# Optimization experiments

Measured on AMD Instinct MI355X. Metric: run time of the kernel, lower is better.

Reference implementation:

```python
import jax, jax.numpy as jnp
import numpy as np

D_MODEL = 768
N_HEADS = 4
D_HEAD = D_MODEL // N_HEADS
EPS = 1e-3  # keras LayerNormalization default


def gelu_tanh(x):
    return 0.5 * x * (1.0 + jnp.tanh(np.sqrt(2.0 / np.pi) * (x + 0.044715 * x ** 3)))


def layer_norm(x, g, b):
    mu = jnp.mean(x, axis=-1, keepdims=True)
    var = jnp.mean(jnp.square(x - mu), axis=-1, keepdims=True)
    return (x - mu) * jax.lax.rsqrt(var + EPS) * g + b


def setup_inputs() -> dict:
    key = jax.random.key(0)
    ks = jax.random.split(key, 12)
    B, S = 8, 1024
    x = jax.random.normal(ks[0], (B, S, D_MODEL), dtype=jnp.float32)
    # causal mask: 1 on strictly-future positions (added as mask * -1e9)
    mask = jnp.triu(jnp.ones((S, S), dtype=jnp.float32), k=1)[None, None]
    s = 0.02
    params = {
        'W1': jax.random.normal(ks[1], (D_MODEL, 3 * D_MODEL)) * s,
        'b1': jnp.zeros((3 * D_MODEL,), jnp.float32),
        'W3': jax.random.normal(ks[2], (D_MODEL, D_MODEL)) * s,
        'b3': jnp.zeros((D_MODEL,), jnp.float32),
        'W2': jax.random.normal(ks[3], (D_MODEL, 4 * D_MODEL)) * s,
        'b2': jnp.zeros((4 * D_MODEL,), jnp.float32),
        'W4': jax.random.normal(ks[4], (4 * D_MODEL, D_MODEL)) * s,
        'b4': jnp.zeros((D_MODEL,), jnp.float32),
        'g1': jnp.ones((D_MODEL,), jnp.float32),
        'be1': jnp.zeros((D_MODEL,), jnp.float32),
        'g2': jnp.ones((D_MODEL,), jnp.float32),
        'be2': jnp.zeros((D_MODEL,), jnp.float32),
    }
    return {'x': x, 'mask': mask, **params}


def reference(x, mask, W1, b1, W3, b3, W2, b2, W4, b4, g1, be1, g2, be2):
    B, S, _ = x.shape
    xn = layer_norm(x, g1, be1)
    qkv = xn @ W1 + b1                                  # [B,S,3D]
    q, k, v = jnp.split(qkv, 3, axis=-1)
    def split_heads(t):
        return t.reshape(B, S, N_HEADS, D_HEAD).transpose(0, 2, 1, 3)  # [B,H,S,dh]
    q, k, v = map(split_heads, (q, k, v))
    present = jnp.stack([k, v], axis=1)                  # [B,2,H,S,dh]
    w = jnp.einsum('bhqd,bhkd->bhqk', q, k)
    # NOTE: source divides by rsqrt(d_head) => multiplies by sqrt(d_head) (faithful bug)
    w = w * jnp.sqrt(jnp.float32(D_HEAD))
    w = w + mask * -1e9
    w = jax.nn.softmax(w, axis=-1)
    attn = jnp.einsum('bhqk,bhkd->bhqd', w, v)           # [B,H,S,dh]
    attn = attn.transpose(0, 2, 1, 3).reshape(B, S, D_MODEL)
    x = attn @ W3 + b3 + x                               # residual 1
    xn2 = layer_norm(x, g2, be2)
    h = gelu_tanh(xn2 @ W2 + b2)                         # [B,S,4D]
    x = h @ W4 + b4 + x                                  # residual 2
    return x, present
```

## Files before the change

kernel.cpp:

```cpp
#include <hip/hip_runtime.h>
#include <hip/hip_bf16.h>
#include <cstdint>

#define D_MODEL 768
#define NH 4
#define DH 192
#define SEQ 1024
#define BATCH 8

typedef __bf16 bf16x8 __attribute__((ext_vector_type(8)));
typedef float floatx4 __attribute__((ext_vector_type(4)));

__device__ __forceinline__ float bf2f(ushort u) {
    union { uint32_t i; float f; } x; x.i = ((uint32_t)u) << 16; return x.f;
}
__device__ __forceinline__ ushort f2bf(float f) {
    union { float f; uint32_t i; } x; x.f = f;
    uint32_t i = x.i;
    uint32_t r = (i + 0x7FFFu + ((i >> 16) & 1u)) >> 16;
    return (ushort)r;
}

__device__ __forceinline__ void gl_lds16(const void* g, void* l) {
    __builtin_amdgcn_global_load_lds(
        (const __attribute__((address_space(1))) uint32_t*)g,
        (__attribute__((address_space(3))) uint32_t*)l, 16, 0, 0);
}

template <int SPLIT>
__global__ void ln_kernel(const float* __restrict__ x, const float* __restrict__ g,
                          const float* __restrict__ be,
                          ushort* __restrict__ y_hi, ushort* __restrict__ y_lo) {
    int row = blockIdx.x;
    int tid = threadIdx.x;
    const float* xr = x + (size_t)row * D_MODEL;
    float v[3];
    float s = 0.f, ss = 0.f;
#pragma unroll
    for (int i = 0; i < 3; i++) {
        float t = xr[tid + i * 256];
        v[i] = t; s += t; ss += t * t;
    }
#pragma unroll
    for (int off = 32; off > 0; off >>= 1) {
        s += __shfl_down(s, off);
        ss += __shfl_down(ss, off);
    }
    __shared__ float rs[4], rss[4];
    int wid = tid >> 6;
    if ((tid & 63) == 0) { rs[wid] = s; rss[wid] = ss; }
    __syncthreads();
    s = rs[0] + rs[1] + rs[2] + rs[3];
    ss = rss[0] + rss[1] + rss[2] + rss[3];
    float mu = s * (1.f / 768.f);
    float var = ss * (1.f / 768.f) - mu * mu;
    float rstd = rsqrtf(var + 1e-3f);
#pragma unroll
    for (int i = 0; i < 3; i++) {
        int d = tid + i * 256;
        float val = (v[i] - mu) * rstd * g[d] + be[d];
        ushort hi = f2bf(val);
        y_hi[(size_t)row * D_MODEL + d] = hi;
        if (SPLIT) y_lo[(size_t)row * D_MODEL + d] = f2bf(val - bf2f(hi));
    }
}

__global__ void transpose_kernel(const float* __restrict__ W, ushort* __restrict__ Wt,
                                 int K, int N) {
    __shared__ ushort tile[64][65];
    int nt = N >> 6;
    int bk = blockIdx.x / nt, bn = blockIdx.x % nt;
    int tid = threadIdx.x;
#pragma unroll
    for (int i = 0; i < 16; i++) {
        int lin = i * 256 + tid; int r = lin >> 6, c = lin & 63;
        tile[r][c] = f2bf(W[(size_t)(bk * 64 + r) * N + bn * 64 + c]);
    }
    __syncthreads();
#pragma unroll
    for (int i = 0; i < 16; i++) {
        int lin = i * 256 + tid; int r = lin >> 6, c = lin & 63;
        Wt[(size_t)(bn * 64 + r) * K + bk * 64 + c] = tile[c][r];
    }
}

__global__ void transpose_split_kernel(const float* __restrict__ W,
                                       ushort* __restrict__ Wt_hi, ushort* __restrict__ Wt_lo,
                                       int K, int N) {
    __shared__ ushort th[64][65];
    __shared__ ushort tl[64][65];
    int nt = N >> 6;
    int bk = blockIdx.x / nt, bn = blockIdx.x % nt;
    int tid = threadIdx.x;
#pragma unroll
    for (int i = 0; i < 16; i++) {
        int lin = i * 256 + tid; int r = lin >> 6, c = lin & 63;
        float v = W[(size_t)(bk * 64 + r) * N + bn * 64 + c];
        ushort hi = f2bf(v);
        th[r][c] = hi;
        tl[r][c] = f2bf(v - bf2f(hi));
    }
    __syncthreads();
#pragma unroll
    for (int i = 0; i < 16; i++) {
        int lin = i * 256 + tid; int r = lin >> 6, c = lin & 63;
        size_t o = (size_t)(bn * 64 + r) * K + bk * 64 + c;
        Wt_hi[o] = th[c][r];
        Wt_lo[o] = tl[c][r];
    }
}

__global__ __launch_bounds__(256, 2) void gemm_qkv_split(
    const ushort* __restrict__ Ah, const ushort* __restrict__ Al,
    const ushort* __restrict__ Bh, const ushort* __restrict__ Bl,
    const float* __restrict__ bias,
    float* __restrict__ Qf, float* __restrict__ present,
    ushort* __restrict__ Khg, ushort* __restrict__ Klg, ushort* __restrict__ Vtg) {
    const int K = 768;
    __shared__ __align__(16) __bf16 sAh[2][128][32];
    __shared__ __align__(16) __bf16 sAl[2][128][32];
    __shared__ __align__(16) __bf16 sBh[2][128][32];
    __shared__ __align__(16) __bf16 sBl[2][128][32];
    int tid = threadIdx.x;
    int rowBase = blockIdx.y << 7;
    int colBase = blockIdx.x << 7;
    int wave = tid >> 6, lane = tid & 63;
    int wm = (wave & 1) << 6, wn = (wave >> 1) << 6;
    int lrow = lane & 15, q = lane >> 4;
    int lkswz = ((q ^ ((lrow >> 1) & 3)) << 3);
    floatx4 acc[4][4] = {};

    int srow = lane >> 2;
    int schunk = (lane & 3) ^ ((lane >> 3) & 3);
    const ushort* Ah0 = Ah + (size_t)(rowBase + wave * 32 + srow) * K + schunk * 8;
    const ushort* Al0 = Al + (size_t)(rowBase + wave * 32 + srow) * K + schunk * 8;
    const ushort* Bh0 = Bh + (size_t)(colBase + wave * 32 + srow) * K + schunk * 8;
    const ushort* Bl0 = Bl + (size_t)(colBase + wave * 32 + srow) * K + schunk * 8;
    const size_t r16 = (size_t)16 * K;
    int wr = wave * 32;

    gl_lds16(Ah0, &sAh[0][wr][0]);       gl_lds16(Ah0 + r16, &sAh[0][wr + 16][0]);
    gl_lds16(Al0, &sAl[0][wr][0]);       gl_lds16(Al0 + r16, &sAl[0][wr + 16][0]);
    gl_lds16(Bh0, &sBh[0][wr][0]);       gl_lds16(Bh0 + r16, &sBh[0][wr + 16][0]);
    gl_lds16(Bl0, &sBl[0][wr][0]);       gl_lds16(Bl0 + r16, &sBl[0][wr + 16][0]);
    __syncthreads();

    const int nt = K >> 5;
    for (int t = 0; t < nt; t++) {
        int cur = t & 1, nb = cur ^ 1;
        if (t + 1 < nt) {
            int k0 = (t + 1) << 5;
            gl_lds16(Ah0 + k0, &sAh[nb][wr][0]);  gl_lds16(Ah0 + r16 + k0, &sAh[nb][wr + 16][0]);
            gl_lds16(Al0 + k0, &sAl[nb][wr][0]);  gl_lds16(Al0 + r16 + k0, &sAl[nb][wr + 16][0]);
            gl_lds16(Bh0 + k0, &sBh[nb][wr][0]);  gl_lds16(Bh0 + r16 + k0, &sBh[nb][wr + 16][0]);
            gl_lds16(Bl0 + k0, &sBl[nb][wr][0]);  gl_lds16(Bl0 + r16 + k0, &sBl[nb][wr + 16][0]);
        }
        bf16x8 afh[4], afl[4], bvh[4], bvl[4];
#pragma unroll
        for (int i = 0; i < 4; i++) {
            afh[i] = *(const bf16x8*)&sAh[cur][wm + i * 16 + lrow][lkswz];
            afl[i] = *(const bf16x8*)&sAl[cur][wm + i * 16 + lrow][lkswz];
        }
#pragma unroll
        for (int jj = 0; jj < 4; jj++) {
            bvh[jj] = *(const bf16x8*)&sBh[cur][wn + jj * 16 + lrow][lkswz];
            bvl[jj] = *(const bf16x8*)&sBl[cur][wn + jj * 16 + lrow][lkswz];
        }
#pragma unroll
        for (int i = 0; i < 4; i++)
#pragma unroll
            for (int jj = 0; jj < 4; jj++) {
                acc[i][jj] = __builtin_amdgcn_mfma_f32_16x16x32_bf16(afh[i], bvh[jj], acc[i][jj], 0, 0, 0);
                acc[i][jj] = __builtin_amdgcn_mfma_f32_16x16x32_bf16(afh[i], bvl[jj], acc[i][jj], 0, 0, 0);
                acc[i][jj] = __builtin_amdgcn_mfma_f32_16x16x32_bf16(afl[i], bvh[jj], acc[i][jj], 0, 0, 0);
            }
        __syncthreads();
    }

    int cr = (lane >> 4) << 2;
    int cc = lane & 15;
#pragma unroll
    for (int jj = 0; jj < 4; jj++) {
        int col = colBase + wn + jj * 16 + cc;
        float bvs = bias[col];
        if (colBase < 768) {
#pragma unroll
            for (int i = 0; i < 4; i++) {
                int row0 = rowBase + wm + i * 16 + cr;
#pragma unroll
                for (int r = 0; r < 4; r++)
                    Qf[(size_t)(row0 + r) * 768 + col] = acc[i][jj][r] + bvs;
            }
        } else if (colBase < 1536) {
            int kc = col - 768;
            int h = kc / DH, d = kc - h * DH;
#pragma unroll
            for (int i = 0; i < 4; i++) {
                int row0 = rowBase + wm + i * 16 + cr;
#pragma unroll
                for (int r = 0; r < 4; r++) {
                    int row = row0 + r;
                    int b = row >> 10, s = row & 1023;
                    float v = acc[i][jj][r] + bvs;
                    present[((size_t)((b * 2) * NH + h) * SEQ + s) * DH + d] = v;
                    ushort hi = f2bf(v);
                    Khg[(size_t)row * 768 + kc] = hi;
                    Klg[(size_t)row * 768 + kc] = f2bf(v - bf2f(hi));
                }
            }
        } else {
            int vc = col - 1536;
            int h = vc / DH, d = vc - h * DH;
#pragma unroll
            for (int i = 0; i < 4; i++) {
                int row0 = rowBase + wm + i * 16 + cr;
#pragma unroll
                for (int r = 0; r < 4; r++) {
                    int row = row0 + r;
                    int b = row >> 10, s = row & 1023;
                    float v = acc[i][jj][r] + bvs;
                    present[((size_t)((b * 2 + 1) * NH + h) * SEQ + s) * DH + d] = v;
                    Vtg[((size_t)b * 768 + vc) * 1024 + s] = f2bf(v);
                }
            }
        }
    }
}

template <int GELU, int RES, int OUTF32>
__global__ __launch_bounds__(256, 4) void gemm_bt(
    const ushort* __restrict__ A, const ushort* __restrict__ Bt,
    const float* __restrict__ bias, const float* __restrict__ resid,
    void* __restrict__ Cout, int M, int N, int K) {
    __shared__ __align__(16) __bf16 sA[2][128][32];
    __shared__ __align__(16) __bf16 sB[2][128][32];
    int tid = threadIdx.x;
    int rowBase = blockIdx.y << 7;
    int colBase = blockIdx.x << 7;
    int wave = tid >> 6, lane = tid & 63;
    int wm = (wave & 1) << 6, wn = (wave >> 1) << 6;
    int lrow = lane & 15, q = lane >> 4;
    int lkswz = ((q ^ ((lrow >> 1) & 3)) << 3);
    floatx4 acc[4][4] = {};

    int srow = lane >> 2;
    int schunk = (lane & 3) ^ ((lane >> 3) & 3);
    const ushort* Ag0 = A + (size_t)(rowBase + wave * 32 + srow) * K + schunk * 8;
    const ushort* Bg0 = Bt + (size_t)(colBase + wave * 32 + srow) * K + schunk * 8;
    const size_t r16 = (size_t)16 * K;
    int wr = wave * 32;

    gl_lds16(Ag0, &sA[0][wr][0]);  gl_lds16(Ag0 + r16, &sA[0][wr + 16][0]);
    gl_lds16(Bg0, &sB[0][wr][0]);  gl_lds16(Bg0 + r16, &sB[0][wr + 16][0]);
    __syncthreads();

    int nt = K >> 5;
    for (int t = 0; t < nt; t++) {
        int cur = t & 1, nb = cur ^ 1;
        if (t + 1 < nt) {
            int k0 = (t + 1) << 5;
            gl_lds16(Ag0 + k0, &sA[nb][wr][0]);  gl_lds16(Ag0 + r16 + k0, &sA[nb][wr + 16][0]);
            gl_lds16(Bg0 + k0, &sB[nb][wr][0]);  gl_lds16(Bg0 + r16 + k0, &sB[nb][wr + 16][0]);
        }
        bf16x8 af[4], bv[4];
#pragma unroll
        for (int i = 0; i < 4; i++) af[i] = *(const bf16x8*)&sA[cur][wm + i * 16 + lrow][lkswz];
#pragma unroll
        for (int jj = 0; jj < 4; jj++) bv[jj] = *(const bf16x8*)&sB[cur][wn + jj * 16 + lrow][lkswz];
#pragma unroll
        for (int i = 0; i < 4; i++)
#pragma unroll
            for (int jj = 0; jj < 4; jj++)
                acc[i][jj] = __builtin_amdgcn_mfma_f32_16x16x32_bf16(af[i], bv[jj], acc[i][jj], 0, 0, 0);
        __syncthreads();
    }
    int cr = (lane >> 4) << 2;
    int cc = lane & 15;
#pragma unroll
    for (int jj = 0; jj < 4; jj++) {
        int col = colBase + wn + jj * 16 + cc;
        float bvs = bias[col];
#pragma unroll
        for (int i = 0; i < 4; i++) {
            int row0 = rowBase + wm + i * 16 + cr;
#pragma unroll
            for (int r = 0; r < 4; r++) {
                int row = row0 + r;
                float v = acc[i][jj][r] + bvs;
                if (GELU) {
                    float u = v;
                    float z2 = -1.5957691216057308f * (u + 0.044715f * u * u * u);
                    v = u / (1.f + __expf(z2));
                }
                if (RES) v += resid[(size_t)row * N + col];
                if (OUTF32) ((float*)Cout)[(size_t)row * N + col] = v;
                else ((ushort*)Cout)[(size_t)row * N + col] = f2bf(v);
            }
        }
    }
}

__global__ __launch_bounds__(512, 2) void attn_flash(
    const float* __restrict__ Qf, const ushort* __restrict__ Khg,
    const ushort* __restrict__ Klg, const ushort* __restrict__ Vtg,
    ushort* __restrict__ attn2) {
    int bi = blockIdx.x;
    int j = bi & 7;
    int h = (bi >> 3) & 3;
    int b = bi >> 5;
    int tid = threadIdx.x;
    int wave = tid >> 6, lane = tid & 63;
    int l15 = lane & 15, quad = lane >> 4;
    int tile = (wave < 4) ? (15 - j) : j;
    int w16 = wave & 3;
    int s0 = tile << 6;
    int its = 2 * (15 - j) + 2;
    int myKt = (s0 + w16 * 16 + 15) >> 5;

    __shared__ __align__(16) __bf16 sKh[2][32][200];
    __shared__ __align__(16) __bf16 sKl[2][32][200];
    __shared__ __align__(16) __bf16 sVt[2][192][40];
    __shared__ __align__(16) ushort sP[8][16][40];

    const bool lo_half = (tid < 256);
    const int kr0 = tid / 24, ke0 = (tid % 24) * 8;
    const int c1 = lo_half ? (512 + tid) : (256 + tid);
    const int kr1 = c1 / 24, ke1 = (c1 % 24) * 8;
    const int vd0 = tid >> 2, ve0 = (tid & 3) * 8;
    const int vd1 = (512 + tid) >> 2, ve1 = ((512 + tid) & 3) * 8;

    const ushort* Khb = Khg + (size_t)(b * 1024) * 768 + h * 192;
    const ushort* Klb = Klg + (size_t)(b * 1024) * 768 + h * 192;
    const ushort* Vtb = Vtg + ((size_t)(b * 768) + h * 192) * 1024;
    const ushort* Bb = lo_half ? Khb : Klb;
    __bf16* pKB = lo_half ? &sKh[0][kr1][ke1] : &sKl[0][kr1][ke1];

    uint4 rA, rB, rC, rD, rE;

    rA = *(const uint4*)(Khb + (size_t)kr0 * 768 + ke0);
    rC = *(const uint4*)(Klb + (size_t)kr0 * 768 + ke0);
    rB = *(const uint4*)(Bb + (size_t)kr1 * 768 + ke1);
    rD = *(const uint4*)(Vtb + (size_t)vd0 * 1024 + ve0);
    if (lo_half) rE = *(const uint4*)(Vtb + (size_t)vd1 * 1024 + ve1);

    bf16x8 qh[6], ql[6];
    {
        int qrow = s0 + w16 * 16 + l15;
        const float* qp = Qf + (size_t)(b * SEQ + qrow) * 768 + h * DH + quad * 8;
#pragma unroll
        for (int dt = 0; dt < 6; dt++) {
            float4 v0 = *(const float4*)(qp + dt * 32);
            float4 v1 = *(const float4*)(qp + dt * 32 + 4);
            float vv[8] = {v0.x, v0.y, v0.z, v0.w, v1.x, v1.y, v1.z, v1.w};
            bf16x8 hh, ll;
#pragma unroll
            for (int jj = 0; jj < 8; jj++) {
                float sv = vv[jj] * 13.856406460551018f;
                ushort hu = f2bf(sv);
                ((ushort*)&hh)[jj] = hu;
                ((ushort*)&ll)[jj] = f2bf(sv - bf2f(hu));
            }
            qh[dt] = hh; ql[dt] = ll;
        }
    }

    floatx4 O[12] = {};
    float m_run[4], l_run[4];
#pragma unroll
    for (int r = 0; r < 4; r++) { m_run[r] = -1e30f; l_run[r] = 0.f; }

    *(uint4*)&sKh[0][kr0][ke0] = rA;
    *(uint4*)&sKl[0][kr0][ke0] = rC;
    *(uint4*)(pKB) = rB;
    *(uint4*)&sVt[0][vd0][ve0] = rD;
    if (lo_half) *(uint4*)&sVt[0][vd1][ve1] = rE;
    __syncthreads();

    for (int kt = 0; kt < its; kt++) {
        int cur = kt & 1;
        bool pfetch = (kt + 1 < its);
        if (pfetch) {
            int koff = (kt + 1) * 32;
            rA = *(const uint4*)(Khb + (size_t)(koff + kr0) * 768 + ke0);
            rC = *(const uint4*)(Klb + (size_t)(koff + kr0) * 768 + ke0);
            rB = *(const uint4*)(Bb + (size_t)(koff + kr1) * 768 + ke1);
            rD = *(const uint4*)(Vtb + (size_t)vd0 * 1024 + koff + ve0);
            if (lo_half) rE = *(const uint4*)(Vtb + (size_t)vd1 * 1024 + koff + ve1);
        }
        if (kt <= myKt) {
            floatx4 S0 = {}, S1 = {};
#pragma unroll
            for (int dt = 0; dt < 6; dt++) {
                bf16x8 k0h = *(const bf16x8*)&sKh[cur][l15][dt * 32 + quad * 8];
                bf16x8 k0l = *(const bf16x8*)&sKl[cur][l15][dt * 32 + quad * 8];
                bf16x8 k1h = *(const bf16x8*)&sKh[cur][16 + l15][dt * 32 + quad * 8];
                bf16x8 k1l = *(const bf16x8*)&sKl[cur][16 + l15][dt * 32 + quad * 8];
                S0 = __builtin_amdgcn_mfma_f32_16x16x32_bf16(qh[dt], k0h, S0, 0, 0, 0);
                S0 = __builtin_amdgcn_mfma_f32_16x16x32_bf16(qh[dt], k0l, S0, 0, 0, 0);
                S0 = __builtin_amdgcn_mfma_f32_16x16x32_bf16(ql[dt], k0h, S0, 0, 0, 0);
                S1 = __builtin_amdgcn_mfma_f32_16x16x32_bf16(qh[dt], k1h, S1, 0, 0, 0);
                S1 = __builtin_amdgcn_mfma_f32_16x16x32_bf16(qh[dt], k1l, S1, 0, 0, 0);
                S1 = __builtin_amdgcn_mfma_f32_16x16x32_bf16(ql[dt], k1h, S1, 0, 0, 0);
            }
            int qg = s0 + w16 * 16 + quad * 4;
            int colb = kt * 32 + l15;
            float mt[4];
#pragma unroll
            for (int r = 0; r < 4; r++) {
                float a = (colb <= qg + r) ? S0[r] : -1e30f;
                float c = (colb + 16 <= qg + r) ? S1[r] : -1e30f;
                S0[r] = a; S1[r] = c;
                mt[r] = fmaxf(a, c);
            }
#pragma unroll
            for (int m = 1; m <= 8; m <<= 1)
#pragma unroll
                for (int r = 0; r < 4; r++) mt[r] = fmaxf(mt[r], __shfl_xor(mt[r], m));
            float alpha[4], rsum[4], P0[4], P1[4];
#pragma unroll
            for (int r = 0; r < 4; r++) {
                float mn = fmaxf(m_run[r], mt[r]);
                alpha[r] = __expf(m_run[r] - mn);
                m_run[r] = mn;
                P0[r] = __expf(S0[r] - mn);
                P1[r] = __expf(S1[r] - mn);
                rsum[r] = P0[r] + P1[r];
            }
#pragma unroll
            for (int m = 1; m <= 8; m <<= 1)
#pragma unroll
                for (int r = 0; r < 4; r++) rsum[r] += __shfl_xor(rsum[r], m);
#pragma unroll
            for (int r = 0; r < 4; r++) l_run[r] = l_run[r] * alpha[r] + rsum[r];
#pragma unroll
            for (int t = 0; t < 12; t++)
#pragma unroll
                for (int r = 0; r < 4; r++) O[t][r] *= alpha[r];
#pragma unroll
            for (int r = 0; r < 4; r++) {
                sP[wave][quad * 4 + r][l15]      = f2bf(P0[r]);
                sP[wave][quad * 4 + r][16 + l15] = f2bf(P1[r]);
            }
            bf16x8 pfrag = *(const bf16x8*)&sP[wave][l15][quad * 8];
#pragma unroll
            for (int t = 0; t < 12; t++) {
                bf16x8 vf = *(const bf16x8*)&sVt[cur][t * 16 + l15][quad * 8];
                O[t] = __builtin_amdgcn_mfma_f32_16x16x32_bf16(pfrag, vf, O[t], 0, 0, 0);
            }
        }
        if (pfetch) {
            int nb = cur ^ 1;
            *(uint4*)&sKh[nb][kr0][ke0] = rA;
            *(uint4*)&sKl[nb][kr0][ke0] = rC;
            *(uint4*)(pKB + nb * 6400) = rB;
            *(uint4*)&sVt[nb][vd0][ve0] = rD;
            if (lo_half) *(uint4*)&sVt[nb][vd1][ve1] = rE;
        }
        __syncthreads();
    }

    float inv[4];
#pragma unroll
    for (int r = 0; r < 4; r++) inv[r] = 1.f / l_run[r];
    int qrow = s0 + w16 * 16 + quad * 4;
#pragma unroll
    for (int t = 0; t < 12; t++)
#pragma unroll
        for (int r = 0; r < 4; r++)
            attn2[(size_t)(b * SEQ + qrow + r) * D_MODEL + h * DH + t * 16 + l15] =
                f2bf(O[t][r] * inv[r]);
}

extern "C" void kernel_launch(void* const* d_in, const int* in_sizes, int n_in,
                              void* d_out, int out_size, void* d_ws, size_t ws_size,
                              hipStream_t stream) {
    const float* x  = (const float*)d_in[0];
    const float* W1 = (const float*)d_in[2];
    const float* b1 = (const float*)d_in[3];
    const float* W3 = (const float*)d_in[4];
    const float* b3 = (const float*)d_in[5];
    const float* W2 = (const float*)d_in[6];
    const float* b2 = (const float*)d_in[7];
    const float* W4 = (const float*)d_in[8];
    const float* b4 = (const float*)d_in[9];
    const float* g1 = (const float*)d_in[10];
    const float* be1 = (const float*)d_in[11];
    const float* g2 = (const float*)d_in[12];
    const float* be2 = (const float*)d_in[13];

    char* ws = (char*)d_ws;
    ushort* W1t_hi = (ushort*)(ws + 0);
    ushort* W1t_lo = (ushort*)(ws + 3538944);
    ushort* W3t    = (ushort*)(ws + 7077888);
    ushort* W2t    = (ushort*)(ws + 8257536);
    ushort* W4t    = (ushort*)(ws + 12976128);
    ushort* xn_hi  = (ushort*)(ws + 17694720);
    ushort* attn2  = (ushort*)(ws + 17694720);
    ushort* xn_lo  = (ushort*)(ws + 30277632);
    ushort* xn2    = (ushort*)(ws + 30277632);
    float*  Qf     = (float*)(ws + 42860544);
    ushort* hbuf   = (ushort*)(ws + 42860544);
    ushort* Khg    = (ushort*)(ws + 68026368);
    ushort* Klg    = (ushort*)(ws + 80609280);
    ushort* Vtg    = (ushort*)(ws + 93192192);
    float*  x1     = (float*)(ws + 105775104);

    float* out0 = (float*)d_out;
    float* present = out0 + 6291456;

    transpose_split_kernel<<<(768 / 64) * (2304 / 64), 256, 0, stream>>>(W1, W1t_hi, W1t_lo, 768, 2304);
    transpose_kernel<<<(768 / 64) * (768 / 64), 256, 0, stream>>>(W3, W3t, 768, 768);
    transpose_kernel<<<(768 / 64) * (3072 / 64), 256, 0, stream>>>(W2, W2t, 768, 3072);
    transpose_kernel<<<(3072 / 64) * (768 / 64), 256, 0, stream>>>(W4, W4t, 3072, 768);

    ln_kernel<1><<<8192, 256, 0, stream>>>(x, g1, be1, xn_hi, xn_lo);
    gemm_qkv_split<<<dim3(2304 / 128, 8192 / 128), 256, 0, stream>>>(
        xn_hi, xn_lo, W1t_hi, W1t_lo, b1, Qf, present, Khg, Klg, Vtg);
    attn_flash<<<BATCH * NH * 8, 512, 0, stream>>>(Qf, Khg, Klg, Vtg, attn2);
    gemm_bt<0, 1, 1><<<dim3(768 / 128, 8192 / 128), 256, 0, stream>>>(
        attn2, W3t, b3, x, x1, 8192, 768, 768);
    ln_kernel<0><<<8192, 256, 0, stream>>>(x1, g2, be2, xn2, nullptr);
    gemm_bt<1, 0, 0><<<dim3(3072 / 128, 8192 / 128), 256, 0, stream>>>(
        xn2, W2t, b2, nullptr, hbuf, 8192, 3072, 768);
    gemm_bt<0, 1, 1><<<dim3(768 / 128, 8192 / 128), 256, 0, stream>>>(
        hbuf, W4t, b4, x1, out0, 8192, 768, 3072);
}
```

Measured before the change: 513.1 us.

## Single-buffer QKV GEMM for higher occupancy, emit split bf16 Q directly

The QKV GEMM drops LDS double buffering in favour of a single buffer with syncs around each load, and raises launch bounds from 2 to 4 blocks per CU so latency is hidden by more resident waves instead of prefetch. The GEMM epilogue now writes Q as hi/lo bf16 pairs rather than fp32, and the sqrt(d_head) scale moves from Q onto K. The attention kernel then loads ready-made bf16x8 Q fragments instead of converting fp32. This trades explicit load/compute overlap and possible register pressure under the tighter bound for occupancy and less Q traffic and conversion work.

```diff
diff --git a/kernel.cpp b/kernel.cpp
--- a/kernel.cpp
+++ b/kernel.cpp
@@ -110,17 +110,17 @@
     }
 }
 
-__global__ __launch_bounds__(256, 2) void gemm_qkv_split(
+__global__ __launch_bounds__(256, 4) void gemm_qkv_split(
     const ushort* __restrict__ Ah, const ushort* __restrict__ Al,
     const ushort* __restrict__ Bh, const ushort* __restrict__ Bl,
     const float* __restrict__ bias,
-    float* __restrict__ Qf, float* __restrict__ present,
+    ushort* __restrict__ Qhg, ushort* __restrict__ Qlg, float* __restrict__ present,
     ushort* __restrict__ Khg, ushort* __restrict__ Klg, ushort* __restrict__ Vtg) {
     const int K = 768;
-    __shared__ __align__(16) __bf16 sAh[2][128][32];
-    __shared__ __align__(16) __bf16 sAl[2][128][32];
-    __shared__ __align__(16) __bf16 sBh[2][128][32];
-    __shared__ __align__(16) __bf16 sBl[2][128][32];
+    __shared__ __align__(16) __bf16 sAh[128][32];
+    __shared__ __align__(16) __bf16 sAl[128][32];
+    __shared__ __align__(16) __bf16 sBh[128][32];
+    __shared__ __align__(16) __bf16 sBl[128][32];
     int tid = threadIdx.x;
     int rowBase = blockIdx.y << 7;
     int colBase = blockIdx.x << 7;
@@ -139,32 +139,25 @@
     const size_t r16 = (size_t)16 * K;
     int wr = wave * 32;
 
-    gl_lds16(Ah0, &sAh[0][wr][0]);       gl_lds16(Ah0 + r16, &sAh[0][wr + 16][0]);
-    gl_lds16(Al0, &sAl[0][wr][0]);       gl_lds16(Al0 + r16, &sAl[0][wr + 16][0]);
-    gl_lds16(Bh0, &sBh[0][wr][0]);       gl_lds16(Bh0 + r16, &sBh[0][wr + 16][0]);
-    gl_lds16(Bl0, &sBl[0][wr][0]);       gl_lds16(Bl0 + r16, &sBl[0][wr + 16][0]);
-    __syncthreads();
-
     const int nt = K >> 5;
     for (int t = 0; t < nt; t++) {
-        int cur = t & 1, nb = cur ^ 1;
-        if (t + 1 < nt) {
-            int k0 = (t + 1) << 5;
-            gl_lds16(Ah0 + k0, &sAh[nb][wr][0]);  gl_lds16(Ah0 + r16 + k0, &sAh[nb][wr + 16][0]);
-            gl_lds16(Al0 + k0, &sAl[nb][wr][0]);  gl_lds16(Al0 + r16 + k0, &sAl[nb][wr + 16][0]);
-            gl_lds16(Bh0 + k0, &sBh[nb][wr][0]);  gl_lds16(Bh0 + r16 + k0, &sBh[nb][wr + 16][0]);
-            gl_lds16(Bl0 + k0, &sBl[nb][wr][0]);  gl_lds16(Bl0 + r16 + k0, &sBl[nb][wr + 16][0]);
-        }
+        if (t) __syncthreads();
+        int k0 = t << 5;
+        gl_lds16(Ah0 + k0, &sAh[wr][0]);  gl_lds16(Ah0 + r16 + k0, &sAh[wr + 16][0]);
+        gl_lds16(Al0 + k0, &sAl[wr][0]);  gl_lds16(Al0 + r16 + k0, &sAl[wr + 16][0]);
+        gl_lds16(Bh0 + k0, &sBh[wr][0]);  gl_lds16(Bh0 + r16 + k0, &sBh[wr + 16][0]);
+        gl_lds16(Bl0 + k0, &sBl[wr][0]);  gl_lds16(Bl0 + r16 + k0, &sBl[wr + 16][0]);
+        __syncthreads();
         bf16x8 afh[4], afl[4], bvh[4], bvl[4];
 #pragma unroll
         for (int i = 0; i < 4; i++) {
-            afh[i] = *(const bf16x8*)&sAh[cur][wm + i * 16 + lrow][lkswz];
-            afl[i] = *(const bf16x8*)&sAl[cur][wm + i * 16 + lrow][lkswz];
+            afh[i] = *(const bf16x8*)&sAh[wm + i * 16 + lrow][lkswz];
+            afl[i] = *(const bf16x8*)&sAl[wm + i * 16 + lrow][lkswz];
         }
 #pragma unroll
         for (int jj = 0; jj < 4; jj++) {
-            bvh[jj] = *(const bf16x8*)&sBh[cur][wn + jj * 16 + lrow][lkswz];
-            bvl[jj] = *(const bf16x8*)&sBl[cur][wn + jj * 16 + lrow][lkswz];
+            bvh[jj] = *(const bf16x8*)&sBh[wn + jj * 16 + lrow][lkswz];
+            bvl[jj] = *(const bf16x8*)&sBl[wn + jj * 16 + lrow][lkswz];
         }
 #pragma unroll
         for (int i = 0; i < 4; i++)
@@ -174,7 +167,6 @@
                 acc[i][jj] = __builtin_amdgcn_mfma_f32_16x16x32_bf16(afh[i], bvl[jj], acc[i][jj], 0, 0, 0);
                 acc[i][jj] = __builtin_amdgcn_mfma_f32_16x16x32_bf16(afl[i], bvh[jj], acc[i][jj], 0, 0, 0);
             }
-        __syncthreads();
     }
 
     int cr = (lane >> 4) << 2;
@@ -188,8 +180,12 @@
             for (int i = 0; i < 4; i++) {
                 int row0 = rowBase + wm + i * 16 + cr;
 #pragma unroll
-                for (int r = 0; r < 4; r++)
-                    Qf[(size_t)(row0 + r) * 768 + col] = acc[i][jj][r] + bvs;
+                for (int r = 0; r < 4; r++) {
+                    float v = acc[i][jj][r] + bvs;
+                    ushort hi = f2bf(v);
+                    Qhg[(size_t)(row0 + r) * 768 + col] = hi;
+                    Qlg[(size_t)(row0 + r) * 768 + col] = f2bf(v - bf2f(hi));
+                }
             }
         } else if (colBase < 1536) {
             int kc = col - 768;
@@ -203,9 +199,10 @@
                     int b = row >> 10, s = row & 1023;
                     float v = acc[i][jj][r] + bvs;
                     present[((size_t)((b * 2) * NH + h) * SEQ + s) * DH + d] = v;
-                    ushort hi = f2bf(v);
+                    float sv = v * 13.856406460551018f;
+                    ushort hi = f2bf(sv);
                     Khg[(size_t)row * 768 + kc] = hi;
-                    Klg[(size_t)row * 768 + kc] = f2bf(v - bf2f(hi));
+                    Klg[(size_t)row * 768 + kc] = f2bf(sv - bf2f(hi));
                 }
             }
         } else {
@@ -301,9 +298,9 @@
 }
 
 __global__ __launch_bounds__(512, 2) void attn_flash(
-    const float* __restrict__ Qf, const ushort* __restrict__ Khg,
-    const ushort* __restrict__ Klg, const ushort* __restrict__ Vtg,
-    ushort* __restrict__ attn2) {
+    const ushort* __restrict__ Qhg, const ushort* __restrict__ Qlg,
+    const ushort* __restrict__ Khg, const ushort* __restrict__ Klg,
+    const ushort* __restrict__ Vtg, ushort* __restrict__ attn2) {
     int bi = blockIdx.x;
     int j = bi & 7;
     int h = (bi >> 3) & 3;
@@ -346,21 +343,12 @@
     bf16x8 qh[6], ql[6];
     {
         int qrow = s0 + w16 * 16 + l15;
-        const float* qp = Qf + (size_t)(b * SEQ + qrow) * 768 + h * DH + quad * 8;
+        const ushort* qph = Qhg + (size_t)(b * SEQ + qrow) * 768 + h * DH + quad * 8;
+        const ushort* qpl = Qlg + (size_t)(b * SEQ + qrow) * 768 + h * DH + quad * 8;
 #pragma unroll
         for (int dt = 0; dt < 6; dt++) {
-            float4 v0 = *(const float4*)(qp + dt * 32);
-            float4 v1 = *(const float4*)(qp + dt * 32 + 4);
-            float vv[8] = {v0.x, v0.y, v0.z, v0.w, v1.x, v1.y, v1.z, v1.w};
-            bf16x8 hh, ll;
-#pragma unroll
-            for (int jj = 0; jj < 8; jj++) {
-                float sv = vv[jj] * 13.856406460551018f;
-                ushort hu = f2bf(sv);
-                ((ushort*)&hh)[jj] = hu;
-                ((ushort*)&ll)[jj] = f2bf(sv - bf2f(hu));
-            }
-            qh[dt] = hh; ql[dt] = ll;
+            qh[dt] = *(const bf16x8*)(qph + dt * 32);
+            ql[dt] = *(const bf16x8*)(qpl + dt * 32);
         }
     }
 
@@ -498,7 +486,8 @@
     ushort* attn2  = (ushort*)(ws + 17694720);
     ushort* xn_lo  = (ushort*)(ws + 30277632);
     ushort* xn2    = (ushort*)(ws + 30277632);
-    float*  Qf     = (float*)(ws + 42860544);
+    ushort* Qhg    = (ushort*)(ws + 42860544);
+    ushort* Qlg    = (ushort*)(ws + 55443456);
     ushort* hbuf   = (ushort*)(ws + 42860544);
     ushort* Khg    = (ushort*)(ws + 68026368);
     ushort* Klg    = (ushort*)(ws + 80609280);
@@ -515,8 +504,8 @@
 
     ln_kernel<1><<<8192, 256, 0, stream>>>(x, g1, be1, xn_hi, xn_lo);
     gemm_qkv_split<<<dim3(2304 / 128, 8192 / 128), 256, 0, stream>>>(
-        xn_hi, xn_lo, W1t_hi, W1t_lo, b1, Qf, present, Khg, Klg, Vtg);
-    attn_flash<<<BATCH * NH * 8, 512, 0, stream>>>(Qf, Khg, Klg, Vtg, attn2);
+        xn_hi, xn_lo, W1t_hi, W1t_lo, b1, Qhg, Qlg, present, Khg, Klg, Vtg);
+    attn_flash<<<BATCH * NH * 8, 512, 0, stream>>>(Qhg, Qlg, Khg, Klg, Vtg, attn2);
     gemm_bt<0, 1, 1><<<dim3(768 / 128, 8192 / 128), 256, 0, stream>>>(
         attn2, W3t, b3, x, x1, 8192, 768, 768);
     ln_kernel<0><<<8192, 256, 0, stream>>>(x1, g2, be2, xn2, nullptr);
```

New measurement: 526.5 us. 2.6% more time.
